# Performance work log

Hardware: AMD Instinct MI355X
Metric: run time of the kernel (lower is better)

The kernel has to match this reference:

```python
import jax, jax.numpy as jnp
import numpy as np

IN, OUT, B = 8192, 8192, 256

def setup_inputs() -> dict:
    key = jax.random.key(0)
    k1, k2, k3, k4, k5 = jax.random.split(key, 5)
    x = jax.random.normal(k1, (B, IN), dtype=jnp.float32)
    low = jax.random.uniform(k2, (IN,), dtype=jnp.float32, minval=-1.0, maxval=0.0)
    high = low + jax.random.uniform(k3, (IN,), dtype=jnp.float32)  # guarantees low <= high
    W = jax.random.normal(k4, (OUT, IN), dtype=jnp.float32) * 0.02
    b = jax.random.normal(k5, (OUT,), dtype=jnp.float32) * 0.02
    return {"x": x, "low": low, "high": high, "W": W, "b": b}

def reference(x, low, high, W, b):
    # standard linear: x @ W.T + b
    y = jnp.einsum('bi,oi->bo', x, W) + b
    # interval bound propagation: swap bounds where weights are negative.
    # Equivalent to per-row masked matmul loop in the original:
    #   low_out[i]  = (W+[i] @ low) + (W-[i] @ high) + b[i]
    #   high_out[i] = (W+[i] @ high) + (W-[i] @ low) + b[i]
    W_pos = jnp.maximum(W, 0.0)
    W_neg = jnp.minimum(W, 0.0)
    low_out = W_pos @ low + W_neg @ high + b
    high_out = W_pos @ high + W_neg @ low + b
    return (y, low_out, high_out)
```

## Files before the change

kernel.cpp:

```cpp
#include <hip/hip_runtime.h>

#define M_TOTAL 256
#define N_TOTAL 8192
#define K_TOTAL 8192

typedef __attribute__((ext_vector_type(4))) float f32x4;
typedef __attribute__((ext_vector_type(8))) short s16x8;
typedef __attribute__((ext_vector_type(4))) int   i32x4;
typedef unsigned short ushort_t;

__device__ __forceinline__ int pk(float a, float b) {
    return (int)__builtin_amdgcn_perm(__float_as_uint(b), __float_as_uint(a), 0x07060302u);
}

__global__ __launch_bounds__(256)
void prep_kernel(const float* __restrict__ x,
                 const float* __restrict__ low,
                 const float* __restrict__ high,
                 ushort_t* __restrict__ xpre,
                 float* __restrict__ lh,
                 float* __restrict__ hl) {
    const int bx = blockIdx.x, t = threadIdx.x;
    if (bx < 1024) {
        const int id  = bx * 256 + t;
        const int kt  = id >> 11;
        const int c   = (id >> 8) & 7;
        const int row = id & 255;
        const float* src = x + (size_t)row * K_TOTAL + kt * 64 + c * 8;
        f32x4 s0 = *(const f32x4*)(src);
        f32x4 s1 = *(const f32x4*)(src + 4);
        i32x4 bi;
        bi[0] = pk(s0[0], s0[1]); bi[1] = pk(s0[2], s0[3]);
        bi[2] = pk(s1[0], s1[1]); bi[3] = pk(s1[2], s1[3]);
        *(i32x4*)(xpre + (size_t)id * 8) = bi;
    } else {
        const int i = (bx - 1024) * 256 + t;
        float lo = low[i], hi = high[i];
        lh[i] = lo + hi;
        hl[i] = hi - lo;
    }
}

__global__ __launch_bounds__(512)
void abstract_linear_kernel(const ushort_t* __restrict__ xpre,
                            const float* __restrict__ W,
                            const float* __restrict__ lh,
                            const float* __restrict__ hl,
                            const float* __restrict__ bias,
                            float* __restrict__ out) {
    __shared__ float ybuf[M_TOTAL * 32];
    __shared__ float pbuf[4 * 32];
    __shared__ float rbuf[4 * 32];

    const int t    = threadIdx.x;
    const int w    = t >> 6;
    const int nw   = w & 1;
    const int kh   = w >> 1;
    const int lane = t & 63;
    const int l15  = lane & 15;
    const int lq   = lane >> 4;
    const int n0   = blockIdx.x * 32;
    const int nl   = nw * 16 + l15;

    f32x4 acc[16];
#pragma unroll
    for (int i = 0; i < 16; ++i) acc[i] = (f32x4){0.f, 0.f, 0.f, 0.f};

    float P = 0.f, R = 0.f;

    const float*    wp  = W  + (size_t)(n0 + nl) * K_TOTAL + kh * 2048 + lq * 8;
    const float*    lhp = lh + kh * 2048 + lq * 8;
    const float*    hlp = hl + kh * 2048 + lq * 8;
    const ushort_t* ap  = xpre + (size_t)kh * 64 * 8192 + lq * 2048 + l15 * 8;

    f32x4 wA[2], wB[2], lA[2], lB[2], hA[2], hB[2];

    auto ldW = [&](int sl, int st) {
        wA[sl] = *(const f32x4*)(wp  + st * 32);
        wB[sl] = *(const f32x4*)(wp  + st * 32 + 4);
        lA[sl] = *(const f32x4*)(lhp + st * 32);
        lB[sl] = *(const f32x4*)(lhp + st * 32 + 4);
        hA[sl] = *(const f32x4*)(hlp + st * 32);
        hB[sl] = *(const f32x4*)(hlp + st * 32 + 4);
    };

    auto compute = [&](int sl, int st) {
        f32x4 w0 = wA[sl], w1 = wB[sl];
        i32x4 bi;
        bi[0] = pk(w0[0], w0[1]); bi[1] = pk(w0[2], w0[3]);
        bi[2] = pk(w1[0], w1[1]); bi[3] = pk(w1[2], w1[3]);
        s16x8 bf = *(s16x8*)&bi;
        f32x4 l0 = lA[sl], l1 = lB[sl], h0 = hA[sl], h1 = hB[sl];
#pragma unroll
        for (int e = 0; e < 4; ++e) {
            P = fmaf(w0[e], l0[e], P);
            P = fmaf(w1[e], l1[e], P);
            R = fmaf(fabsf(w0[e]), h0[e], R);
            R = fmaf(fabsf(w1[e]), h1[e], R);
        }
        const ushort_t* a_st = ap + (size_t)st * 8192;
#pragma unroll
        for (int half = 0; half < 2; ++half) {
            s16x8 af[8];
#pragma unroll
            for (int mi = 0; mi < 8; ++mi)
                af[mi] = *(const s16x8*)(a_st + (half * 8 + mi) * 128);
#pragma unroll
            for (int mi = 0; mi < 8; ++mi)
                acc[half * 8 + mi] = __builtin_amdgcn_mfma_f32_16x16x32_bf16(
                    af[mi], bf, acc[half * 8 + mi], 0, 0, 0);
        }
    };

    ldW(0, 0);
    for (int st = 0; st < 64; st += 2) {
        ldW(1, st + 1);
        compute(0, st);
        if (st < 62) ldW(0, st + 2);
        compute(1, st + 1);
    }

    P += __shfl_xor(P, 16); P += __shfl_xor(P, 32);
    R += __shfl_xor(R, 16); R += __shfl_xor(R, 32);
    if (lane < 16) {
        pbuf[kh * 32 + nl] = P;
        rbuf[kh * 32 + nl] = R;
    }

    const float bv = bias[n0 + nl];

    for (int rr = 0; rr < 4; ++rr) {
        __syncthreads();
        if (kh == rr) {
#pragma unroll
            for (int mi = 0; mi < 16; ++mi) {
#pragma unroll
                for (int e = 0; e < 4; ++e) {
                    int m = mi * 16 + lq * 4 + e;
                    int idx = m * 32 + nl;
                    float v = acc[mi][e];
                    if (rr > 0) v += ybuf[idx];
                    if (rr < 3) ybuf[idx] = v;
                    else out[(size_t)m * N_TOTAL + n0 + nl] = v + bv;
                }
            }
        }
    }
    __syncthreads();

    if (w == 0 && lane < 32) {
        float Ps = pbuf[lane] + pbuf[32 + lane] + pbuf[64 + lane] + pbuf[96 + lane];
        float Rs = rbuf[lane] + rbuf[32 + lane] + rbuf[64 + lane] + rbuf[96 + lane];
        float bb = bias[n0 + lane];
        out[(size_t)M_TOTAL * N_TOTAL + n0 + lane]           = 0.5f * (Ps - Rs) + bb;
        out[(size_t)M_TOTAL * N_TOTAL + N_TOTAL + n0 + lane] = 0.5f * (Ps + Rs) + bb;
    }
}

extern "C" void kernel_launch(void* const* d_in, const int* in_sizes, int n_in,
                              void* d_out, int out_size, void* d_ws, size_t ws_size,
                              hipStream_t stream) {
    const float* x    = (const float*)d_in[0];
    const float* low  = (const float*)d_in[1];
    const float* high = (const float*)d_in[2];
    const float* W    = (const float*)d_in[3];
    const float* b    = (const float*)d_in[4];
    float* out = (float*)d_out;

    ushort_t* xpre = (ushort_t*)d_ws;
    float* lh = (float*)((char*)d_ws + (size_t)M_TOTAL * K_TOTAL * 2);
    float* hl = lh + K_TOTAL;

    hipLaunchKernelGGL(prep_kernel, dim3(1056), dim3(256), 0, stream,
                       x, low, high, xpre, lh, hl);
    hipLaunchKernelGGL(abstract_linear_kernel, dim3(N_TOTAL / 32), dim3(512), 0, stream,
                       xpre, W, lh, hl, b, out);
}
```

Baseline: 484.1 us.

## Split K eight ways with each wave computing both N-halves to reuse A fragments

Each of the eight waves now owns a 1024-wide K slice and computes both 16-column halves of the 32-column tile. One A fragment load therefore feeds two MFMAs, halving global A traffic per MFMA. The lh/hl loads move out of the double buffer and are read directly, and launch bounds ask for two blocks per CU. In exchange the accumulator register count doubles (128 floats), which risks spills under the occupancy hint, and the serial cross-wave reduction through shared memory grows from four rounds to eight.

New measurement: 543.5 us. 12.3% more time.

```diff
diff --git a/kernel.cpp b/kernel.cpp
--- a/kernel.cpp
+++ b/kernel.cpp
@@ -41,7 +41,7 @@
     }
 }
 
-__global__ __launch_bounds__(512)
+__global__ __launch_bounds__(512, 2)
 void abstract_linear_kernel(const ushort_t* __restrict__ xpre,
                             const float* __restrict__ W,
                             const float* __restrict__ lh,
@@ -49,54 +49,60 @@
                             const float* __restrict__ bias,
                             float* __restrict__ out) {
     __shared__ float ybuf[M_TOTAL * 32];
-    __shared__ float pbuf[4 * 32];
-    __shared__ float rbuf[4 * 32];
+    __shared__ float pbuf[8 * 32];
+    __shared__ float rbuf[8 * 32];
 
     const int t    = threadIdx.x;
-    const int w    = t >> 6;
-    const int nw   = w & 1;
-    const int kh   = w >> 1;
+    const int kh   = t >> 6;
     const int lane = t & 63;
     const int l15  = lane & 15;
     const int lq   = lane >> 4;
     const int n0   = blockIdx.x * 32;
-    const int nl   = nw * 16 + l15;
-
-    f32x4 acc[16];
-#pragma unroll
-    for (int i = 0; i < 16; ++i) acc[i] = (f32x4){0.f, 0.f, 0.f, 0.f};
-
-    float P = 0.f, R = 0.f;
-
-    const float*    wp  = W  + (size_t)(n0 + nl) * K_TOTAL + kh * 2048 + lq * 8;
-    const float*    lhp = lh + kh * 2048 + lq * 8;
-    const float*    hlp = hl + kh * 2048 + lq * 8;
-    const ushort_t* ap  = xpre + (size_t)kh * 64 * 8192 + lq * 2048 + l15 * 8;
-
-    f32x4 wA[2], wB[2], lA[2], lB[2], hA[2], hB[2];
+
+    f32x4 acc[16][2];
+#pragma unroll
+    for (int i = 0; i < 16; ++i) {
+        acc[i][0] = (f32x4){0.f, 0.f, 0.f, 0.f};
+        acc[i][1] = (f32x4){0.f, 0.f, 0.f, 0.f};
+    }
+
+    float P0 = 0.f, P1 = 0.f, R0 = 0.f, R1 = 0.f;
+
+    const float*    wp0 = W + (size_t)(n0 + l15) * K_TOTAL + kh * 1024 + lq * 8;
+    const float*    wp1 = wp0 + (size_t)16 * K_TOTAL;
+    const float*    lhp = lh + kh * 1024 + lq * 8;
+    const float*    hlp = hl + kh * 1024 + lq * 8;
+    const ushort_t* ap  = xpre + (size_t)(kh * 128 + lq) * 2048 + l15 * 8;
+
+    f32x4 wreg[2][4];
 
     auto ldW = [&](int sl, int st) {
-        wA[sl] = *(const f32x4*)(wp  + st * 32);
-        wB[sl] = *(const f32x4*)(wp  + st * 32 + 4);
-        lA[sl] = *(const f32x4*)(lhp + st * 32);
-        lB[sl] = *(const f32x4*)(lhp + st * 32 + 4);
-        hA[sl] = *(const f32x4*)(hlp + st * 32);
-        hB[sl] = *(const f32x4*)(hlp + st * 32 + 4);
+        wreg[sl][0] = *(const f32x4*)(wp0 + st * 32);
+        wreg[sl][1] = *(const f32x4*)(wp0 + st * 32 + 4);
+        wreg[sl][2] = *(const f32x4*)(wp1 + st * 32);
+        wreg[sl][3] = *(const f32x4*)(wp1 + st * 32 + 4);
     };
 
     auto compute = [&](int sl, int st) {
-        f32x4 w0 = wA[sl], w1 = wB[sl];
-        i32x4 bi;
-        bi[0] = pk(w0[0], w0[1]); bi[1] = pk(w0[2], w0[3]);
-        bi[2] = pk(w1[0], w1[1]); bi[3] = pk(w1[2], w1[3]);
-        s16x8 bf = *(s16x8*)&bi;
-        f32x4 l0 = lA[sl], l1 = lB[sl], h0 = hA[sl], h1 = hB[sl];
+        f32x4 w0A = wreg[sl][0], w0B = wreg[sl][1];
+        f32x4 w1A = wreg[sl][2], w1B = wreg[sl][3];
+        i32x4 b0, b1;
+        b0[0] = pk(w0A[0], w0A[1]); b0[1] = pk(w0A[2], w0A[3]);
+        b0[2] = pk(w0B[0], w0B[1]); b0[3] = pk(w0B[2], w0B[3]);
+        b1[0] = pk(w1A[0], w1A[1]); b1[1] = pk(w1A[2], w1A[3]);
+        b1[2] = pk(w1B[0], w1B[1]); b1[3] = pk(w1B[2], w1B[3]);
+        s16x8 bf0 = *(s16x8*)&b0;
+        s16x8 bf1 = *(s16x8*)&b1;
+        f32x4 lA = *(const f32x4*)(lhp + st * 32);
+        f32x4 lB = *(const f32x4*)(lhp + st * 32 + 4);
+        f32x4 hA = *(const f32x4*)(hlp + st * 32);
+        f32x4 hB = *(const f32x4*)(hlp + st * 32 + 4);
 #pragma unroll
         for (int e = 0; e < 4; ++e) {
-            P = fmaf(w0[e], l0[e], P);
-            P = fmaf(w1[e], l1[e], P);
-            R = fmaf(fabsf(w0[e]), h0[e], R);
-            R = fmaf(fabsf(w1[e]), h1[e], R);
+            P0 = fmaf(w0A[e], lA[e], P0); P0 = fmaf(w0B[e], lB[e], P0);
+            R0 = fmaf(fabsf(w0A[e]), hA[e], R0); R0 = fmaf(fabsf(w0B[e]), hB[e], R0);
+            P1 = fmaf(w1A[e], lA[e], P1); P1 = fmaf(w1B[e], lB[e], P1);
+            R1 = fmaf(fabsf(w1A[e]), hA[e], R1); R1 = fmaf(fabsf(w1B[e]), hB[e], R1);
         }
         const ushort_t* a_st = ap + (size_t)st * 8192;
 #pragma unroll
@@ -106,54 +112,70 @@
             for (int mi = 0; mi < 8; ++mi)
                 af[mi] = *(const s16x8*)(a_st + (half * 8 + mi) * 128);
 #pragma unroll
-            for (int mi = 0; mi < 8; ++mi)
-                acc[half * 8 + mi] = __builtin_amdgcn_mfma_f32_16x16x32_bf16(
-                    af[mi], bf, acc[half * 8 + mi], 0, 0, 0);
+            for (int mi = 0; mi < 8; ++mi) {
+                acc[half * 8 + mi][0] = __builtin_amdgcn_mfma_f32_16x16x32_bf16(
+                    af[mi], bf0, acc[half * 8 + mi][0], 0, 0, 0);
+                acc[half * 8 + mi][1] = __builtin_amdgcn_mfma_f32_16x16x32_bf16(
+                    af[mi], bf1, acc[half * 8 + mi][1], 0, 0, 0);
+            }
         }
     };
 
     ldW(0, 0);
-    for (int st = 0; st < 64; st += 2) {
+    for (int st = 0; st < 32; st += 2) {
         ldW(1, st + 1);
         compute(0, st);
-        if (st < 62) ldW(0, st + 2);
+        if (st < 30) ldW(0, st + 2);
         compute(1, st + 1);
     }
 
-    P += __shfl_xor(P, 16); P += __shfl_xor(P, 32);
-    R += __shfl_xor(R, 16); R += __shfl_xor(R, 32);
+    P0 += __shfl_xor(P0, 16); P0 += __shfl_xor(P0, 32);
+    P1 += __shfl_xor(P1, 16); P1 += __shfl_xor(P1, 32);
+    R0 += __shfl_xor(R0, 16); R0 += __shfl_xor(R0, 32);
+    R1 += __shfl_xor(R1, 16); R1 += __shfl_xor(R1, 32);
     if (lane < 16) {
-        pbuf[kh * 32 + nl] = P;
-        rbuf[kh * 32 + nl] = R;
-    }
-
-    const float bv = bias[n0 + nl];
-
-    for (int rr = 0; rr < 4; ++rr) {
+        pbuf[kh * 32 + l15]      = P0;
+        pbuf[kh * 32 + 16 + l15] = P1;
+        rbuf[kh * 32 + l15]      = R0;
+        rbuf[kh * 32 + 16 + l15] = R1;
+    }
+
+    const float bv0 = bias[n0 + l15];
+    const float bv1 = bias[n0 + 16 + l15];
+
+    for (int rr = 0; rr < 8; ++rr) {
         __syncthreads();
         if (kh == rr) {
 #pragma unroll
             for (int mi = 0; mi < 16; ++mi) {
 #pragma unroll
                 for (int e = 0; e < 4; ++e) {
-                    int m = mi * 16 + lq * 4 + e;
-                    int idx = m * 32 + nl;
-                    float v = acc[mi][e];
-                    if (rr > 0) v += ybuf[idx];
-                    if (rr < 3) ybuf[idx] = v;
-                    else out[(size_t)m * N_TOTAL + n0 + nl] = v + bv;
+                    int m  = mi * 16 + lq * 4 + e;
+                    int i0 = m * 32 + l15;
+                    float v0 = acc[mi][0][e];
+                    float v1 = acc[mi][1][e];
+                    if (rr > 0) { v0 += ybuf[i0]; v1 += ybuf[i0 + 16]; }
+                    if (rr < 7) { ybuf[i0] = v0; ybuf[i0 + 16] = v1; }
+                    else {
+                        out[(size_t)m * N_TOTAL + n0 + l15]      = v0 + bv0;
+                        out[(size_t)m * N_TOTAL + n0 + 16 + l15] = v1 + bv1;
+                    }
                 }
             }
         }
     }
     __syncthreads();
 
-    if (w == 0 && lane < 32) {
-        float Ps = pbuf[lane] + pbuf[32 + lane] + pbuf[64 + lane] + pbuf[96 + lane];
-        float Rs = rbuf[lane] + rbuf[32 + lane] + rbuf[64 + lane] + rbuf[96 + lane];
-        float bb = bias[n0 + lane];
-        out[(size_t)M_TOTAL * N_TOTAL + n0 + lane]           = 0.5f * (Ps - Rs) + bb;
-        out[(size_t)M_TOTAL * N_TOTAL + N_TOTAL + n0 + lane] = 0.5f * (Ps + Rs) + bb;
+    if (t < 32) {
+        float Ps = 0.f, Rs = 0.f;
+#pragma unroll
+        for (int k = 0; k < 8; ++k) {
+            Ps += pbuf[k * 32 + t];
+            Rs += rbuf[k * 32 + t];
+        }
+        float bb = bias[n0 + t];
+        out[(size_t)M_TOTAL * N_TOTAL + n0 + t]           = 0.5f * (Ps - Rs) + bb;
+        out[(size_t)M_TOTAL * N_TOTAL + N_TOTAL + n0 + t] = 0.5f * (Ps + Rs) + bb;
     }
 }
 
```
